# Performance work log

Hardware: AMD Instinct MI355X
Metric: run time of the kernel (lower is better)

Reference implementation:

```python
import jax, jax.numpy as jnp
import numpy as np

NUM_CLASSES = 80
ALPHA = 1.0
BETA = 6.0
EPS = 1e-9      # assigner eps
IOU_EPS = 1e-7  # bbox_iou eps


def _iou_xyxy(b1, b2):
    # b1: (B, A, 1, 4), b2: (B, 1, M, 4) -> IoU (B, A, M); matches bbox_iou(xywh=False)
    b1x1, b1y1, b1x2, b1y2 = (b1[..., 0], b1[..., 1], b1[..., 2], b1[..., 3])
    b2x1, b2y1, b2x2, b2y2 = (b2[..., 0], b2[..., 1], b2[..., 2], b2[..., 3])
    w1, h1 = b1x2 - b1x1, b1y2 - b1y1 + IOU_EPS
    w2, h2 = b2x2 - b2x1, b2y2 - b2y1 + IOU_EPS
    iw = jnp.clip(jnp.minimum(b1x2, b2x2) - jnp.maximum(b1x1, b2x1), 0)
    ih = jnp.clip(jnp.minimum(b1y2, b2y2) - jnp.maximum(b1y1, b2y1), 0)
    inter = iw * ih
    union = w1 * h1 + w2 * h2 - inter + IOU_EPS
    return inter / union


def _select_highest_overlaps(mask_pos, overlaps, M):
    # Always apply the dedup branch; it is a no-op when no anchor has >1 gt.
    fg = mask_pos.sum(-1)                                   # (B, A)
    multi = fg > 1
    is_max = jax.nn.one_hot(overlaps.argmax(-1), M, dtype=mask_pos.dtype)  # (B, A, M)
    mask_pos = jnp.where(multi[..., None], is_max, mask_pos)
    fg = mask_pos.sum(-1)
    tgt = mask_pos.argmax(-1).astype(jnp.int32)             # (B, A)
    return tgt, fg, mask_pos


def _forward(pd_scores, pd_bboxes, anc_points, gt_labels, gt_bboxes, mask_gt):
    B, A, C = pd_scores.shape
    M = gt_bboxes.shape[1]
    f = pd_scores.dtype
    mgt_b = mask_gt.astype(bool)                            # (B, M)
    mgt_f = mask_gt.astype(f)

    # --- box metrics ---
    overlaps = jnp.clip(_iou_xyxy(pd_bboxes[:, :, None, :], gt_bboxes[:, None, :, :]), 0)  # (B,A,M)
    idx = jnp.broadcast_to(gt_labels[:, None, :].astype(jnp.int32), (B, A, M))
    cls_scores = jnp.take_along_axis(pd_scores, idx, axis=-1)                              # (B,A,M)
    align_metric = cls_scores ** ALPHA * overlaps ** BETA

    # --- anchors inside gt boxes ---
    lt = anc_points[None, :, None, :] - gt_bboxes[:, None, :, :2]   # (B,A,M,2)
    rb = gt_bboxes[:, None, :, 2:] - anc_points[None, :, None, :]
    mask_in_gts = jnp.concatenate([lt, rb], -1).min(-1) > EPS       # (B,A,M) bool
    mask_pos = mask_in_gts.astype(f) * mgt_f[:, None, :]

    # --- fix 1 (vectorized: each (b,gt) iteration only touches its own column) ---
    need1 = mgt_b & (mask_pos.sum(1) == 0)                          # (B,M)
    has_in = mask_in_gts.any(1)                                     # (B,M)
    best1 = jnp.where(has_in, (overlaps * mask_in_gts).argmax(1), overlaps.argmax(1))  # (B,M)
    oh1 = jax.nn.one_hot(best1, A, dtype=f).transpose(0, 2, 1)      # (B,A,M)
    mask_pos = jnp.maximum(mask_pos, oh1 * need1[:, None, :].astype(f))

    tgt, fg, mask_pos = _select_highest_overlaps(mask_pos, overlaps, M)

    # --- fix 2: sequential per-gt reassignment (order-dependent -> lax.scan) ---
    anchor_ids = jnp.arange(A)
    gt_ids = jnp.arange(M)

    def step(carry, g):
        mp, tgi, fgm = carry
        assigned = jnp.any((fgm > 0) & (tgi == g), axis=1)          # (B,)
        need = jnp.take(mgt_b, g, axis=1) & (~assigned)             # (B,)
        best = jnp.take(overlaps, g, axis=2).argmax(1)              # (B,)
        oh_b = anchor_ids[None, :] == best[:, None]                 # (B,A) bool
        upd = need[:, None] & oh_b                                  # (B,A)
        col = (gt_ids == g)[None, None, :]
        mp = jnp.where(upd[:, :, None] & col, jnp.asarray(1, mp.dtype), mp)
        tgi = jnp.where(upd, g, tgi)
        fgm = jnp.where(upd, jnp.asarray(1, fgm.dtype), fgm)
        return (mp, tgi, fgm), None

    (mask_pos, tgt, fg), _ = jax.lax.scan(step, (mask_pos, tgt, fg), jnp.arange(M, dtype=jnp.int32))
    tgt, fg, mask_pos = _select_highest_overlaps(mask_pos, overlaps, M)

    # --- targets ---
    tl = jnp.take_along_axis(gt_labels.astype(jnp.int32), tgt, axis=1)   # (B,A)
    tl = jnp.clip(tl, 0, NUM_CLASSES)
    tb = jnp.take_along_axis(gt_bboxes, tgt[..., None], axis=1)          # (B,A,4)
    ts = jax.nn.one_hot(tl, C, dtype=f)                                  # (B,A,C)
    ts = jnp.where(fg[..., None] > 0, ts, jnp.asarray(0, f))

    # --- normalize scores by task-aligned metric ---
    am = align_metric * mask_pos
    pam = am.max(-1, keepdims=True)                                      # (B,A,1)
    pov = (overlaps * mask_pos).max(-1, keepdims=True)
    norm = (am * pov / (pam + EPS)).max(-1, keepdims=True)               # (B,A,1)
    ts = ts * norm
    return tl, tb, ts, fg > 0, tgt


def setup_inputs() -> dict:
    key = jax.random.key(0)
    B, C, M, IMG = 32, NUM_CLASSES, 32, 640
    ks = jax.random.split(key, 8)
    # YOLO-style anchor grid: strides 8/16/32 -> 80^2 + 40^2 + 20^2 = 8400 points
    pts = []
    for s in (8, 16, 32):
        n = IMG // s
        xs = (np.arange(n, dtype=np.float32) + 0.5) * s
        gy, gx = np.meshgrid(xs, xs, indexing="ij")
        pts.append(np.stack([gx.ravel(), gy.ravel()], -1))
    anc_points = jnp.asarray(np.concatenate(pts, 0))                     # (8400, 2)
    A = anc_points.shape[0]
    pd_scores = jax.random.uniform(ks[0], (B, A, C), dtype=jnp.float32)  # sigmoid-like scores
    wh_p = jax.random.uniform(ks[1], (B, A, 2), minval=16.0, maxval=256.0)
    ctr_p = anc_points[None] + jax.random.normal(ks[2], (B, A, 2)) * 8.0
    pd_bboxes = jnp.concatenate([ctr_p - wh_p / 2, ctr_p + wh_p / 2], -1)
    ctr_g = jax.random.uniform(ks[3], (B, M, 2), minval=60.0, maxval=580.0)
    wh_g = jax.random.uniform(ks[4], (B, M, 2), minval=24.0, maxval=240.0)
    gt_bboxes = jnp.concatenate([ctr_g - wh_g / 2, ctr_g + wh_g / 2], -1)
    gt_labels = jax.random.randint(ks[5], (B, M), 0, C, dtype=jnp.int32)
    n_gt = jax.random.randint(ks[6], (B, 1), 1, M + 1)
    mask_gt = jnp.arange(M)[None, :] < n_gt                              # (B, M) bool
    return dict(pd_scores=pd_scores, pd_bboxes=pd_bboxes, anc_points=anc_points,
                gt_labels=gt_labels, gt_bboxes=gt_bboxes, mask_gt=mask_gt)


def reference(pd_scores, pd_bboxes, anc_points, gt_labels, gt_bboxes, mask_gt):
    return _forward(pd_scores, pd_bboxes, anc_points, gt_labels, gt_bboxes, mask_gt)
```

## Files before the change

### kernel.cpp

```cpp
#include <hip/hip_runtime.h>


#define EPS_IN   1e-9f
#define IOU_EPS  1e-7f

__device__ __forceinline__ float iou_pair(const float4 p, const float4 g) {
#pragma clang fp contract(off)
    float w1 = p.z - p.x;
    float h1 = (p.w - p.y) + IOU_EPS;
    float w2 = g.z - g.x;
    float h2 = (g.w - g.y) + IOU_EPS;
    float iw = fminf(p.z, g.z) - fmaxf(p.x, g.x);
    iw = fmaxf(iw, 0.0f);
    float ih = fminf(p.w, g.w) - fmaxf(p.y, g.y);
    ih = fmaxf(ih, 0.0f);
    float inter = iw * ih;
    float uni = w1 * h1 + w2 * h2 - inter + IOU_EPS;
    float r = inter / uni;
    return fmaxf(r, 0.0f);
}

__device__ __forceinline__ int detect_mode(const void* mg, int nw) {
    const unsigned* w = (const unsigned*)mg;
    int lane = threadIdx.x & 63;
    int badI = 0, badF = 0;
    for (int i = lane; i < nw; i += 64) {
        unsigned v = w[i];
        badI |= (v > 1u);
        badF |= (v != 0u && v != 0x3F800000u);
    }
    unsigned long long bI = __ballot(badI != 0);
    unsigned long long bF = __ballot(badF != 0);
    return bI ? (bF ? 2 : 1) : 0;
}

__device__ __forceinline__ bool mask_at(const void* mg, int mode, int idx) {
    if (mode == 0) return ((const int*)mg)[idx] != 0;
    if (mode == 1) return ((const float*)mg)[idx] != 0.0f;
    return ((const unsigned char*)mg)[idx] != 0;
}

__global__ void k_col(const float4* __restrict__ pdb, const float2* __restrict__ anc,
                      const float4* __restrict__ gtb, const void* mg, int nw,
                      unsigned long long* __restrict__ colKey,
                      unsigned char* __restrict__ needByte,
                      int* __restrict__ cnt, int A, int M) {
    int b = blockIdx.y, m = blockIdx.x, tid = threadIdx.x;
    if (tid == 0) cnt[b * M + m] = 0;
    int mode = detect_mode(mg, nw);
    if (!mask_at(mg, mode, b * M + m)) return;
    float4 g = gtb[b * M + m];
    size_t bA = (size_t)b * A;
    unsigned long long key = 0ull;
    int hasin = 0;
    for (int a = tid; a < A; a += 256) {
        float v = iou_pair(pdb[bA + a], g);
        unsigned long long k =
            ((unsigned long long)__float_as_uint(v) << 32) | (0xFFFFFFFFu - (unsigned)a);
        if (k > key) key = k;
        float2 an = anc[a];
        float mn = fminf(fminf(an.x - g.x, an.y - g.y), fminf(g.z - an.x, g.w - an.y));
        hasin |= (mn > EPS_IN);
    }
    __shared__ unsigned long long skey[4];
    __shared__ int sin_[4];
    int lane = tid & 63, wid = tid >> 6;
    for (int off = 32; off; off >>= 1) {
        unsigned long long o = __shfl_down(key, off);
        if (o > key) key = o;
        hasin |= __shfl_down(hasin, off);
    }
    if (lane == 0) { skey[wid] = key; sin_[wid] = hasin; }
    __syncthreads();
    if (tid == 0) {
        for (int i = 1; i < 4; i++) { if (skey[i] > key) key = skey[i]; hasin |= sin_[i]; }
        colKey[b * M + m] = key;
        needByte[b * M + m] = hasin ? 0 : 1;
    }
}

__global__ void k_sel(const float4* __restrict__ pdb, const float2* __restrict__ anc,
                      const float4* __restrict__ gtb, const void* mg, int nw,
                      const unsigned long long* __restrict__ colKey,
                      const unsigned char* __restrict__ needByte,
                      unsigned* __restrict__ rowbits, int* __restrict__ tgtfg,
                      int* __restrict__ cnt, int A, int M) {
    int b = blockIdx.y, tid = threadIdx.x;
    int a = blockIdx.x * 256 + tid;
    int mode = detect_mode(mg, nw);
    __shared__ float4 sg[32];
    __shared__ unsigned char smg[32];
    __shared__ int fixA[32];
    __shared__ unsigned char fixG[32];
    __shared__ int sL;
    __shared__ int shist[32];
    if (tid < M) {
        sg[tid]  = gtb[b * M + tid];
        smg[tid] = mask_at(mg, mode, b * M + tid) ? 1 : 0;
    }
    if (tid < 32) shist[tid] = 0;
    __syncthreads();
    if (tid < 64) {
        bool needv = (tid < M) && smg[tid] && needByte[b * M + tid];
        unsigned nb = (unsigned)__ballot(needv);
        if (needv) {
            unsigned long long key = colKey[b * M + tid];
            int best = (int)(0xFFFFFFFFu - (unsigned)(key & 0xFFFFFFFFull));
            int pos = __popc(nb & ((1u << tid) - 1u));
            fixA[pos] = best; fixG[pos] = (unsigned char)tid;
        }
        if (tid == 0) sL = __popc(nb);
    }
    __syncthreads();
    size_t bA = (size_t)b * A;
    if (a < A) {
        float2 an = anc[a];
        unsigned bits = 0u;
        for (int m = 0; m < M; m++) {
            float4 g = sg[m];
            float mn = fminf(fminf(an.x - g.x, an.y - g.y), fminf(g.z - an.x, g.w - an.y));
            if (mn > EPS_IN && smg[m]) bits |= (1u << m);
        }
        int L = sL;
        for (int j = 0; j < L; j++) if (fixA[j] == a) bits |= (1u << fixG[j]);
        rowbits[bA + a] = bits;
        int pc = __popc(bits);
        int t;
        if (pc > 1) {
            float4 p = pdb[bA + a];
            float bv = -1.0f; int bm = 0;
            for (int m = 0; m < M; m++) {
                float v = iou_pair(p, sg[m]);
                if (v > bv) { bv = v; bm = m; }
            }
            t = bm;
        } else if (pc == 1) t = __ffs(bits) - 1;
        else t = -1;
        tgtfg[bA + a] = t;
        if (t >= 0) atomicAdd(&shist[t], 1);
    }
    __syncthreads();
    if (tid < 32 && shist[tid]) atomicAdd(&cnt[b * M + tid], shist[tid]);
}

__global__ void k_fix2(const void* mg, int nw,
                       const unsigned long long* __restrict__ colKey,
                       const int* __restrict__ cnt, const int* __restrict__ tgtfg,
                       unsigned* __restrict__ rowbits, int A, int M) {
    int b = blockIdx.x, tid = threadIdx.x;
    int mode = detect_mode(mg, nw);
    size_t bA = (size_t)b * A;
    bool mv = (tid < M) && mask_at(mg, mode, b * M + tid);
    int best = -1;
    if (mv) {
        unsigned long long key = colKey[b * M + tid];
        best = (int)(0xFFFFFFFFu - (unsigned)(key & 0xFFFFFFFFull));
    }
    unsigned maskbits = (unsigned)__ballot(mv);
    int myBest = (tid < 32) ? best : -1;
    int myCnt  = (tid < M && mv) ? cnt[b * M + tid] : 0;
    int myPre  = (myBest >= 0) ? tgtfg[bA + myBest] : -1;
    unsigned myEq = 0u;
    for (int g2 = 0; g2 < 32; g2++) {
        int bb = __shfl(myBest, g2);
        if (bb == myBest) myEq |= (1u << g2);
    }
    unsigned applied = 0u;
    for (int g = 0; g < M; g++) {
        int cg = __shfl(myCnt, g);
        if (((maskbits >> g) & 1u) && cg == 0) {
            int aa      = __shfl(myBest, g);
            unsigned em = __shfl(myEq, g);
            unsigned x  = applied & em;
            int old;
            if (x) old = 31 - __clz(x);
            else   old = __shfl(myPre, g);
            if (tid == old) myCnt--;
            if (tid == g)   myCnt++;
            applied |= (1u << g);
            if (tid == 0)
                atomicOr(&rowbits[bA + aa], 1u << g);
        }
    }
}

__global__ void k_finalts(const float* __restrict__ pds, const float4* __restrict__ pdb,
                          const float4* __restrict__ gtb, const int* __restrict__ gtl,
                          const unsigned* __restrict__ rowbits, float* __restrict__ out,
                          int A, int M, int C, int B) {
    int b = blockIdx.y;
    int base = blockIdx.x * 256;
    int tid = threadIdx.x;
    int a = base + tid;
    __shared__ float4 sg[32];
    __shared__ int slab[32];
    __shared__ float snorm[256];
    __shared__ int stl[256];
    if (tid < M) { sg[tid] = gtb[b * M + tid]; slab[tid] = gtl[b * M + tid]; }
    __syncthreads();
    size_t BA = (size_t)B * A;
    if (a < A) {
        size_t idx = (size_t)b * A + a;
        unsigned bits = rowbits[idx];
        int pc = __popc(bits);
        int tgt, fg; float ov = 0.0f;
        float4 p = pdb[idx];
        if (pc > 1) {
            float bv = -1.0f; int bm = 0;
            for (int m = 0; m < M; m++) {
                float v = iou_pair(p, sg[m]);
                if (v > bv) { bv = v; bm = m; }
            }
            tgt = bm; fg = 1; ov = bv;
        } else if (pc == 1) {
            tgt = __ffs(bits) - 1; fg = 1;
            ov = iou_pair(p, sg[tgt]);
        } else { tgt = 0; fg = 0; }
        int lab = slab[tgt];
        int tl = min(max(lab, 0), C);
        float norm = 0.0f;
        if (fg) {
            int li = (lab >= 0 && lab < C) ? lab : 0;
            float cls = pds[idx * (size_t)C + li];
            float ov6 = powf(ov, 6.0f);
            float v = cls * ov6;
            norm = v * ov / (v + 1e-9f);
        }
        out[idx] = (float)tl;
        ((float4*)(out + BA))[idx] = sg[tgt];
        out[BA * (size_t)(5 + C) + idx] = fg ? 1.0f : 0.0f;
        out[BA * (size_t)(6 + C) + idx] = (float)tgt;
        snorm[tid] = norm;
        stl[tid] = tl;
    }
    __syncthreads();
    int cntA = min(256, A - base);
    int rowf4 = C >> 2;
    int nf4 = cntA * rowf4;
    float4* tsb = (float4*)(out + BA * 5 + ((size_t)b * A + base) * C);
    int q = 256 / rowf4, r = 256 - q * rowf4;
    int row = tid / rowf4;
    int c4  = tid - row * rowf4;
    for (int i = tid; i < nf4; i += 256) {
        float nv = snorm[row];
        int tl   = stl[row];
        int cb = c4 * 4;
        float4 v;
        v.x = (tl == cb + 0) ? nv : 0.0f;
        v.y = (tl == cb + 1) ? nv : 0.0f;
        v.z = (tl == cb + 2) ? nv : 0.0f;
        v.w = (tl == cb + 3) ? nv : 0.0f;
        tsb[i] = v;
        row += q; c4 += r;
        if (c4 >= rowf4) { c4 -= rowf4; row++; }
    }
}

extern "C" void kernel_launch(void* const* d_in, const int* in_sizes, int n_in,
                              void* d_out, int out_size, void* d_ws, size_t ws_size,
                              hipStream_t stream) {
    const float*  pd_scores = (const float*)d_in[0];
    const float4* pd_bboxes = (const float4*)d_in[1];
    const float2* anc       = (const float2*)d_in[2];
    const int*    gt_labels = (const int*)d_in[3];
    const float4* gt_bboxes = (const float4*)d_in[4];
    const void*   mask_gt   = d_in[5];

    int A = in_sizes[2] / 2;
    int B = in_sizes[1] / (A * 4);
    int M = in_sizes[3] / B;
    int C = (int)((long long)in_sizes[0] / ((long long)B * A));
    int nCh = (A + 255) / 256;
    int nw = (B * M) / 4; if (nw > 256) nw = 256;

    char* wp = (char*)d_ws;
    auto carve = [&](size_t bytes) -> char* {
        char* r = wp; wp += (bytes + 255) & ~(size_t)255; return r;
    };
    unsigned* rowbits          = (unsigned*)carve((size_t)B * A * 4);
    int* tgtfg                 = (int*)carve((size_t)B * A * 4);
    unsigned long long* colKey = (unsigned long long*)carve((size_t)B * M * 8);
    int* cnt                   = (int*)carve((size_t)B * M * 4);
    unsigned char* needByte    = (unsigned char*)carve((size_t)B * M);

    float* out = (float*)d_out;

    k_col<<<dim3(M, B), 256, 0, stream>>>(pd_bboxes, anc, gt_bboxes, mask_gt, nw,
                                          colKey, needByte, cnt, A, M);
    k_sel<<<dim3(nCh, B), 256, 0, stream>>>(pd_bboxes, anc, gt_bboxes, mask_gt, nw,
                                            colKey, needByte, rowbits, tgtfg, cnt, A, M);
    k_fix2<<<B, 64, 0, stream>>>(mask_gt, nw, colKey, cnt, tgtfg, rowbits, A, M);
    k_finalts<<<dim3(nCh, B), 256, 0, stream>>>(pd_scores, pd_bboxes, gt_bboxes,
                                                gt_labels, rowbits, out, A, M, C, B);
}
```

Before: 59.94 us.

## Merge column and row passes into one launch, redo fix-ups per block in final kernel

```diff
diff --git a/kernel.cpp b/kernel.cpp
--- a/kernel.cpp
+++ b/kernel.cpp
@@ -40,168 +40,198 @@
     return ((const unsigned char*)mg)[idx] != 0;
 }
 
-__global__ void k_col(const float4* __restrict__ pdb, const float2* __restrict__ anc,
-                      const float4* __restrict__ gtb, const void* mg, int nw,
-                      unsigned long long* __restrict__ colKey,
-                      unsigned char* __restrict__ needByte,
-                      int* __restrict__ cnt, int A, int M) {
-    int b = blockIdx.y, m = blockIdx.x, tid = threadIdx.x;
-    if (tid == 0) cnt[b * M + m] = 0;
-    int mode = detect_mode(mg, nw);
-    if (!mask_at(mg, mode, b * M + m)) return;
-    float4 g = gtb[b * M + m];
-    size_t bA = (size_t)b * A;
-    unsigned long long key = 0ull;
-    int hasin = 0;
-    for (int a = tid; a < A; a += 256) {
-        float v = iou_pair(pdb[bA + a], g);
-        unsigned long long k =
-            ((unsigned long long)__float_as_uint(v) << 32) | (0xFFFFFFFFu - (unsigned)a);
-        if (k > key) key = k;
-        float2 an = anc[a];
-        float mn = fminf(fminf(an.x - g.x, an.y - g.y), fminf(g.z - an.x, g.w - an.y));
-        hasin |= (mn > EPS_IN);
-    }
-    __shared__ unsigned long long skey[4];
-    __shared__ int sin_[4];
-    int lane = tid & 63, wid = tid >> 6;
-    for (int off = 32; off; off >>= 1) {
-        unsigned long long o = __shfl_down(key, off);
-        if (o > key) key = o;
-        hasin |= __shfl_down(hasin, off);
-    }
-    if (lane == 0) { skey[wid] = key; sin_[wid] = hasin; }
-    __syncthreads();
-    if (tid == 0) {
-        for (int i = 1; i < 4; i++) { if (skey[i] > key) key = skey[i]; hasin |= sin_[i]; }
-        colKey[b * M + m] = key;
-        needByte[b * M + m] = hasin ? 0 : 1;
-    }
-}
-
-__global__ void k_sel(const float4* __restrict__ pdb, const float2* __restrict__ anc,
-                      const float4* __restrict__ gtb, const void* mg, int nw,
-                      const unsigned long long* __restrict__ colKey,
-                      const unsigned char* __restrict__ needByte,
-                      unsigned* __restrict__ rowbits, int* __restrict__ tgtfg,
-                      int* __restrict__ cnt, int A, int M) {
+__global__ void k_phase1(const float4* __restrict__ pdb, const float2* __restrict__ anc,
+                         const float4* __restrict__ gtb, const void* mg, int nw,
+                         unsigned long long* __restrict__ colKey,
+                         unsigned char* __restrict__ needByte,
+                         unsigned* __restrict__ rowbits0, short* __restrict__ tgt0,
+                         int* __restrict__ cntChunk,
+                         int A, int M, int nCh) {
     int b = blockIdx.y, tid = threadIdx.x;
-    int a = blockIdx.x * 256 + tid;
-    int mode = detect_mode(mg, nw);
-    __shared__ float4 sg[32];
-    __shared__ unsigned char smg[32];
-    __shared__ int fixA[32];
-    __shared__ unsigned char fixG[32];
-    __shared__ int sL;
-    __shared__ int shist[32];
-    if (tid < M) {
-        sg[tid]  = gtb[b * M + tid];
-        smg[tid] = mask_at(mg, mode, b * M + tid) ? 1 : 0;
-    }
-    if (tid < 32) shist[tid] = 0;
-    __syncthreads();
-    if (tid < 64) {
-        bool needv = (tid < M) && smg[tid] && needByte[b * M + tid];
-        unsigned nb = (unsigned)__ballot(needv);
-        if (needv) {
-            unsigned long long key = colKey[b * M + tid];
-            int best = (int)(0xFFFFFFFFu - (unsigned)(key & 0xFFFFFFFFull));
-            int pos = __popc(nb & ((1u << tid) - 1u));
-            fixA[pos] = best; fixG[pos] = (unsigned char)tid;
-        }
-        if (tid == 0) sL = __popc(nb);
-    }
-    __syncthreads();
-    size_t bA = (size_t)b * A;
-    if (a < A) {
-        float2 an = anc[a];
-        unsigned bits = 0u;
-        for (int m = 0; m < M; m++) {
-            float4 g = sg[m];
-            float mn = fminf(fminf(an.x - g.x, an.y - g.y), fminf(g.z - an.x, g.w - an.y));
-            if (mn > EPS_IN && smg[m]) bits |= (1u << m);
-        }
-        int L = sL;
-        for (int j = 0; j < L; j++) if (fixA[j] == a) bits |= (1u << fixG[j]);
-        rowbits[bA + a] = bits;
-        int pc = __popc(bits);
-        int t;
-        if (pc > 1) {
-            float4 p = pdb[bA + a];
-            float bv = -1.0f; int bm = 0;
-            for (int m = 0; m < M; m++) {
-                float v = iou_pair(p, sg[m]);
-                if (v > bv) { bv = v; bm = m; }
-            }
-            t = bm;
-        } else if (pc == 1) t = __ffs(bits) - 1;
-        else t = -1;
-        tgtfg[bA + a] = t;
-        if (t >= 0) atomicAdd(&shist[t], 1);
-    }
-    __syncthreads();
-    if (tid < 32 && shist[tid]) atomicAdd(&cnt[b * M + tid], shist[tid]);
-}
-
-__global__ void k_fix2(const void* mg, int nw,
-                       const unsigned long long* __restrict__ colKey,
-                       const int* __restrict__ cnt, const int* __restrict__ tgtfg,
-                       unsigned* __restrict__ rowbits, int A, int M) {
-    int b = blockIdx.x, tid = threadIdx.x;
     int mode = detect_mode(mg, nw);
     size_t bA = (size_t)b * A;
-    bool mv = (tid < M) && mask_at(mg, mode, b * M + tid);
-    int best = -1;
-    if (mv) {
-        unsigned long long key = colKey[b * M + tid];
-        best = (int)(0xFFFFFFFFu - (unsigned)(key & 0xFFFFFFFFull));
-    }
-    unsigned maskbits = (unsigned)__ballot(mv);
-    int myBest = (tid < 32) ? best : -1;
-    int myCnt  = (tid < M && mv) ? cnt[b * M + tid] : 0;
-    int myPre  = (myBest >= 0) ? tgtfg[bA + myBest] : -1;
-    unsigned myEq = 0u;
-    for (int g2 = 0; g2 < 32; g2++) {
-        int bb = __shfl(myBest, g2);
-        if (bb == myBest) myEq |= (1u << g2);
-    }
-    unsigned applied = 0u;
-    for (int g = 0; g < M; g++) {
-        int cg = __shfl(myCnt, g);
-        if (((maskbits >> g) & 1u) && cg == 0) {
-            int aa      = __shfl(myBest, g);
-            unsigned em = __shfl(myEq, g);
-            unsigned x  = applied & em;
-            int old;
-            if (x) old = 31 - __clz(x);
-            else   old = __shfl(myPre, g);
-            if (tid == old) myCnt--;
-            if (tid == g)   myCnt++;
-            applied |= (1u << g);
-            if (tid == 0)
-                atomicOr(&rowbits[bA + aa], 1u << g);
-        }
-    }
-}
-
-__global__ void k_finalts(const float* __restrict__ pds, const float4* __restrict__ pdb,
-                          const float4* __restrict__ gtb, const int* __restrict__ gtl,
-                          const unsigned* __restrict__ rowbits, float* __restrict__ out,
-                          int A, int M, int C, int B) {
+
+    if ((int)blockIdx.x < M) {
+        int m = blockIdx.x;
+        if (!mask_at(mg, mode, b * M + m)) return;
+        float4 g = gtb[b * M + m];
+        unsigned long long key = 0ull;
+        int hasin = 0;
+        for (int a = tid; a < A; a += 256) {
+            float v = iou_pair(pdb[bA + a], g);
+            unsigned long long k =
+                ((unsigned long long)__float_as_uint(v) << 32) | (0xFFFFFFFFu - (unsigned)a);
+            if (k > key) key = k;
+            float2 an = anc[a];
+            float mn = fminf(fminf(an.x - g.x, an.y - g.y), fminf(g.z - an.x, g.w - an.y));
+            hasin |= (mn > EPS_IN);
+        }
+        __shared__ unsigned long long skey[4];
+        __shared__ int sin_[4];
+        int lane = tid & 63, wid = tid >> 6;
+        for (int off = 32; off; off >>= 1) {
+            unsigned long long o = __shfl_down(key, off);
+            if (o > key) key = o;
+            hasin |= __shfl_down(hasin, off);
+        }
+        if (lane == 0) { skey[wid] = key; sin_[wid] = hasin; }
+        __syncthreads();
+        if (tid == 0) {
+            for (int i = 1; i < 4; i++) { if (skey[i] > key) key = skey[i]; hasin |= sin_[i]; }
+            colKey[b * M + m] = key;
+            needByte[b * M + m] = hasin ? 0 : 1;
+        }
+    } else {
+        int ch = blockIdx.x - M;
+        int a = ch * 256 + tid;
+        __shared__ float4 sg[32];
+        __shared__ unsigned char smg[32];
+        __shared__ int shist[32];
+        if (tid < M) {
+            sg[tid]  = gtb[b * M + tid];
+            smg[tid] = mask_at(mg, mode, b * M + tid) ? 1 : 0;
+        }
+        if (tid < 32) shist[tid] = 0;
+        __syncthreads();
+        if (a < A) {
+            float2 an = anc[a];
+            unsigned bits = 0u;
+            for (int m = 0; m < M; m++) {
+                float4 g = sg[m];
+                float mn = fminf(fminf(an.x - g.x, an.y - g.y), fminf(g.z - an.x, g.w - an.y));
+                if (mn > EPS_IN && smg[m]) bits |= (1u << m);
+            }
+            rowbits0[bA + a] = bits;
+            int pc = __popc(bits);
+            int t;
+            if (pc > 1) {
+                float4 p = pdb[bA + a];
+                float bv = -1.0f; int bm = 0;
+                for (int m = 0; m < M; m++) {
+                    float v = iou_pair(p, sg[m]);
+                    if (v > bv) { bv = v; bm = m; }
+                }
+                t = bm;
+            } else if (pc == 1) t = __ffs(bits) - 1;
+            else t = -1;
+            tgt0[bA + a] = (short)t;
+            if (t >= 0) atomicAdd(&shist[t], 1);
+        }
+        __syncthreads();
+        if (tid < 32) cntChunk[((size_t)b * nCh + ch) * 32 + tid] = shist[tid];
+    }
+}
+
+__global__ void k_final(const float* __restrict__ pds, const float4* __restrict__ pdb,
+                        const float4* __restrict__ gtb, const int* __restrict__ gtl,
+                        const void* mg, int nw,
+                        const unsigned long long* __restrict__ colKey,
+                        const unsigned char* __restrict__ needByte,
+                        const unsigned* __restrict__ rowbits0,
+                        const short* __restrict__ tgt0,
+                        const int* __restrict__ cntChunk,
+                        float* __restrict__ out,
+                        int A, int M, int C, int B, int nCh) {
     int b = blockIdx.y;
     int base = blockIdx.x * 256;
     int tid = threadIdx.x;
-    int a = base + tid;
+    int mode = detect_mode(mg, nw);
+    size_t bA = (size_t)b * A;
     __shared__ float4 sg[32];
     __shared__ int slab[32];
+    __shared__ int ovrA[64];
+    __shared__ unsigned ovrBits[64];
+    __shared__ int sNov;
     __shared__ float snorm[256];
     __shared__ int stl[256];
     if (tid < M) { sg[tid] = gtb[b * M + tid]; slab[tid] = gtl[b * M + tid]; }
     __syncthreads();
+
+    if (tid < 64) {
+        bool mv = false, needv = false;
+        int best = -1, c0 = 0;
+        if (tid < M) mv = mask_at(mg, mode, b * M + tid);
+        if (mv) {
+            unsigned long long key = colKey[b * M + tid];
+            best = (int)(0xFFFFFFFFu - (unsigned)(key & 0xFFFFFFFFull));
+            needv = (needByte[b * M + tid] != 0);
+        }
+        if (tid < 32) {
+            for (int ch = 0; ch < nCh; ch++)
+                c0 += cntChunk[((size_t)b * nCh + ch) * 32 + tid];
+        }
+        int myPre = (mv && best >= 0) ? (int)tgt0[bA + best] : -1;
+        unsigned maskbits = (unsigned)__ballot(mv);
+        unsigned needBits = (unsigned)__ballot(needv);
+        unsigned myEq = 0u;
+        for (int g2 = 0; g2 < 32; g2++) {
+            int bb = __shfl(best, g2);
+            if (bb == best) myEq |= (1u << g2);
+        }
+        int nov = 0;
+        unsigned rem = needBits;
+        while (rem) {
+            int gl = __ffs(rem) - 1;
+            unsigned em = __shfl(myEq, gl) & needBits;
+            rem &= ~em;
+            int aF = __shfl(best, gl);
+            unsigned addb = em;
+            unsigned bits0 = rowbits0[bA + aF];
+            unsigned bits1 = bits0 | addb;
+            int t1;
+            if (__popc(bits1) > 1) {
+                float4 p = pdb[bA + aF];
+                unsigned long long kk = 0ull;
+                if (tid < M) {
+                    float v = iou_pair(p, sg[tid]);
+                    kk = ((unsigned long long)__float_as_uint(v) << 32) |
+                         (0xFFFFFFFFu - (unsigned)tid);
+                }
+                for (int off = 32; off; off >>= 1) {
+                    unsigned long long o = __shfl_down(kk, off);
+                    if (o > kk) kk = o;
+                }
+                kk = __shfl(kk, 0);
+                t1 = (int)(0xFFFFFFFFu - (unsigned)(kk & 0xFFFFFFFFull));
+            } else {
+                t1 = __ffs(bits1) - 1;
+            }
+            int t0a = __shfl(myPre, gl);
+            if (tid == t0a && t0a >= 0) c0--;
+            if (tid == t1) c0++;
+            if (best == aF) myPre = t1;
+            if (tid == 0) { ovrA[nov] = aF; ovrBits[nov] = addb; }
+            nov++;
+        }
+        unsigned applied = 0u;
+        for (int g = 0; g < M; g++) {
+            int cg = __shfl(c0, g);
+            if (((maskbits >> g) & 1u) && cg == 0) {
+                int aa      = __shfl(best, g);
+                unsigned em = __shfl(myEq, g);
+                unsigned x  = applied & em;
+                int old;
+                if (x) old = 31 - __clz(x);
+                else   old = __shfl(myPre, g);
+                if (tid == old) c0--;
+                if (tid == g)   c0++;
+                applied |= (1u << g);
+                if (tid == 0) { ovrA[nov] = aa; ovrBits[nov] = 1u << g; }
+                nov++;
+            }
+        }
+        if (tid == 0) sNov = nov;
+    }
+    __syncthreads();
+
+    int a = base + tid;
     size_t BA = (size_t)B * A;
+    int nov = sNov;
     if (a < A) {
-        size_t idx = (size_t)b * A + a;
-        unsigned bits = rowbits[idx];
+        size_t idx = bA + a;
+        unsigned bits = rowbits0[idx];
+        for (int j = 0; j < nov; j++)
+            if (ovrA[j] == a) bits |= ovrBits[j];
         int pc = __popc(bits);
         int tgt, fg; float ov = 0.0f;
         float4 p = pdb[idx];
@@ -237,7 +267,7 @@
     int cntA = min(256, A - base);
     int rowf4 = C >> 2;
     int nf4 = cntA * rowf4;
-    float4* tsb = (float4*)(out + BA * 5 + ((size_t)b * A + base) * C);
+    float4* tsb = (float4*)(out + BA * 5 + (bA + base) * C);
     int q = 256 / rowf4, r = 256 - q * rowf4;
     int row = tid / rowf4;
     int c4  = tid - row * rowf4;
@@ -277,19 +307,18 @@
     auto carve = [&](size_t bytes) -> char* {
         char* r = wp; wp += (bytes + 255) & ~(size_t)255; return r;
     };
-    unsigned* rowbits          = (unsigned*)carve((size_t)B * A * 4);
-    int* tgtfg                 = (int*)carve((size_t)B * A * 4);
+    unsigned* rowbits0         = (unsigned*)carve((size_t)B * A * 4);
+    short* tgt0                = (short*)carve((size_t)B * A * 2);
     unsigned long long* colKey = (unsigned long long*)carve((size_t)B * M * 8);
-    int* cnt                   = (int*)carve((size_t)B * M * 4);
     unsigned char* needByte    = (unsigned char*)carve((size_t)B * M);
+    int* cntChunk              = (int*)carve((size_t)B * nCh * 32 * 4);
 
     float* out = (float*)d_out;
 
-    k_col<<<dim3(M, B), 256, 0, stream>>>(pd_bboxes, anc, gt_bboxes, mask_gt, nw,
-                                          colKey, needByte, cnt, A, M);
-    k_sel<<<dim3(nCh, B), 256, 0, stream>>>(pd_bboxes, anc, gt_bboxes, mask_gt, nw,
-                                            colKey, needByte, rowbits, tgtfg, cnt, A, M);
-    k_fix2<<<B, 64, 0, stream>>>(mask_gt, nw, colKey, cnt, tgtfg, rowbits, A, M);
-    k_finalts<<<dim3(nCh, B), 256, 0, stream>>>(pd_scores, pd_bboxes, gt_bboxes,
-                                                gt_labels, rowbits, out, A, M, C, B);
-}
+    k_phase1<<<dim3(M + nCh, B), 256, 0, stream>>>(pd_bboxes, anc, gt_bboxes, mask_gt, nw,
+                                                   colKey, needByte, rowbits0, tgt0,
+                                                   cntChunk, A, M, nCh);
+    k_final<<<dim3(nCh, B), 256, 0, stream>>>(pd_scores, pd_bboxes, gt_bboxes, gt_labels,
+                                              mask_gt, nw, colKey, needByte, rowbits0,
+                                              tgt0, cntChunk, out, A, M, C, B, nCh);
+}
```

Result: faster. 53.33 us (-11.0%).
